# Kernel optimization log

Hardware: AMD Instinct MI355X
Metric: run time of the kernel (lower is better)

## Reference

```python
import jax, jax.numpy as jnp
import numpy as np


def blockdiag_matmul(x, w):
    """Block-diagonal (Monarch) linear: w has shape (nblocks, out_blk, in_blk);
    x has shape (..., nblocks*in_blk); returns (..., nblocks*out_blk)."""
    nb, q, p = w.shape
    lead = x.shape[:-1]
    xb = x.reshape(-1, nb, p)  # (tokens, nblocks, in_blk)
    out = jnp.einsum('bnp,nqp->bnq', xb, w)  # per-block matmul
    return out.reshape(*lead, nb * q)


def setup_inputs() -> dict:
    key = jax.random.key(0)
    k_x, k1, k2, k3 = jax.random.split(key, 4)
    B, S, D = 4, 4096, 2048
    NB, FF = 4, 8192  # nblocks, adjusted intermediate size
    # Kaiming-uniform-like scale for block weights (fan_in = D or FF per block-row)
    s1 = 1.0 / np.sqrt(D)
    s2 = 1.0 / np.sqrt(FF)
    return {
        'x': jax.random.normal(k_x, (B, S, D), dtype=jnp.float32),
        'w1': jax.random.normal(k1, (NB, FF // NB, D // NB), dtype=jnp.float32) * s1,
        'w3': jax.random.normal(k3, (NB, FF // NB, D // NB), dtype=jnp.float32) * s1,
        'w2': jax.random.normal(k2, (NB, D // NB, FF // NB), dtype=jnp.float32) * s2,
    }


def reference(x, w1, w3, w2):
    # SwiGLU MLP: w2(silu(w1(x)) * w3(x)), all projections block-diagonal
    gate = jax.nn.silu(blockdiag_matmul(x, w1))
    up = blockdiag_matmul(x, w3)
    return blockdiag_matmul(gate * up, w2)
```

## Files before the change

kernel.cpp:

```cpp
#include <hip/hip_runtime.h>
#include <cstdint>

typedef __attribute__((ext_vector_type(8))) short bf16x8;
typedef __attribute__((ext_vector_type(4))) float f32x4;
typedef unsigned short u16;

#define RD(p) (*(const bf16x8*)(p))

__device__ inline u16 f2bf(float f) {
  union { float f; unsigned int u; } v; v.f = f;
  unsigned int u = v.u;
  unsigned int r = (u + 0x7fffu + ((u >> 16) & 1u)) >> 16;
  return (u16)r;
}

__device__ inline void gload_lds16(const u16* g, u16* l) {
  __builtin_amdgcn_global_load_lds(
      (const __attribute__((address_space(1))) void*)g,
      (__attribute__((address_space(3))) void*)l, 16, 0, 0);
}

#define PH_BEGIN() \
  __builtin_amdgcn_s_barrier(); \
  asm volatile("s_waitcnt lgkmcnt(0)" ::: "memory"); \
  __builtin_amdgcn_s_setprio(1)
#define PH_END() \
  __builtin_amdgcn_s_setprio(0); \
  __builtin_amdgcn_s_barrier()

__global__ void cvt_f32_bf16(const float* __restrict__ src, u16* __restrict__ dst, int n8) {
  int i = blockIdx.x * blockDim.x + threadIdx.x;
  int stride = gridDim.x * blockDim.x;
  for (; i < n8; i += stride) {
    const float4* s = (const float4*)(src + (size_t)i * 8);
    float4 a = s[0], b = s[1];
    union { u16 h[8]; uint4 v; } o;
    o.h[0] = f2bf(a.x); o.h[1] = f2bf(a.y); o.h[2] = f2bf(a.z); o.h[3] = f2bf(a.w);
    o.h[4] = f2bf(b.x); o.h[5] = f2bf(b.y); o.h[6] = f2bf(b.z); o.h[7] = f2bf(b.w);
    *(uint4*)(dst + (size_t)i * 8) = o.v;
  }
}

__global__ void cvt_w3x(const float* __restrict__ s0, const float* __restrict__ s1,
                        const float* __restrict__ s2, u16* __restrict__ d0,
                        u16* __restrict__ d1, u16* __restrict__ d2) {
  const int n8 = 524288;
  int i = blockIdx.x * blockDim.x + threadIdx.x;
  int stride = gridDim.x * blockDim.x;
  for (; i < 3 * n8; i += stride) {
    int seg = i / n8;
    int j = i - seg * n8;
    const float* src = (seg == 0) ? s0 : (seg == 1) ? s1 : s2;
    u16* dst = (seg == 0) ? d0 : (seg == 1) ? d1 : d2;
    const float4* s = (const float4*)(src + (size_t)j * 8);
    float4 a = s[0], b = s[1];
    union { u16 h[8]; uint4 v; } o;
    o.h[0] = f2bf(a.x); o.h[1] = f2bf(a.y); o.h[2] = f2bf(a.z); o.h[3] = f2bf(a.w);
    o.h[4] = f2bf(b.x); o.h[5] = f2bf(b.y); o.h[6] = f2bf(b.z); o.h[7] = f2bf(b.w);
    *(uint4*)(dst + (size_t)j * 8) = o.v;
  }
}

__launch_bounds__(512, 2)
__global__ void gemm_gateup8(const u16* __restrict__ xb, const u16* __restrict__ w1b,
                             const u16* __restrict__ w3b, u16* __restrict__ hout) {
  constexpr int NT = 8;
  __shared__ __attribute__((aligned(16))) u16 lA[2][256 * 64];
  __shared__ __attribute__((aligned(16))) u16 lB[2][2][128 * 64];

  int bid = blockIdx.x;
  int sw = (bid & 7) * 512 + (bid >> 3);
  int nblk = sw >> 10;
  int rem = sw & 1023;
  int mt = rem >> 4, nt = rem & 15;

  int tid = threadIdx.x, w = tid >> 6, ln = tid & 63;
  int wr = w >> 1, wc = w & 1;
  int l15 = ln & 15, l4 = ln >> 4;
  int lr = ln >> 3, ln8 = ln & 7;

  int cx0 = ((l4 ^ (l15 & 7)) << 4);
  int cx1 = (((4 + l4) ^ (l15 & 7)) << 4);
  int aOff0 = (wr * 64 + l15) * 128 + cx0;
  int aOff1 = (wr * 64 + l15) * 128 + cx1;
  int bOff0 = (wc * 64 + l15) * 128 + cx0;
  int bOff1 = (wc * 64 + l15) * 128 + cx1;

  int u0t = w * 8, u1t = 64 + w * 8;
  int rbA0 = ((u0t >> 5) << 6) + (u0t & 31);
  int rbA1 = ((u1t >> 5) << 6) + (u1t & 31);
  int dA0 = rbA0 * 128, dA1 = rbA1 * 128;
  int dB0 = u0t * 128, dB1 = u1t * 128;
  int gaA0 = rbA0 * 2048, gaA1 = rbA1 * 2048;
  int gaB0 = u0t * 512, gaB1 = u1t * 512;
  int swzg = (ln8 ^ lr) << 3;

  const u16* gA  = xb  + (size_t)(mt * 256) * 2048 + nblk * 512 + lr * 2048 + swzg;
  const u16* gB1 = w1b + (size_t)nblk * (2048 * 512) + (size_t)(nt * 128) * 512 + lr * 512 + swzg;
  const u16* gB3 = w3b + (size_t)nblk * (2048 * 512) + (size_t)(nt * 128) * 512 + lr * 512 + swzg;

  f32x4 acc1[4][4], acc3[4][4];
#pragma unroll
  for (int i = 0; i < 4; i++)
#pragma unroll
    for (int j = 0; j < 4; j++) {
      acc1[i][j] = (f32x4){0.f, 0.f, 0.f, 0.f};
      acc3[i][j] = (f32x4){0.f, 0.f, 0.f, 0.f};
    }

  gload_lds16(gA + gaA0,          (u16*)((char*)lA + dA0));
  gload_lds16(gA + gaA1,          (u16*)((char*)lA + dA1));
  gload_lds16(gB3 + gaB0,         (u16*)((char*)lB + 16384 + dB0));
  gload_lds16(gB3 + gaB1,         (u16*)((char*)lB + 16384 + dB1));
  gload_lds16(gA + gaA0 + 65536,  (u16*)((char*)lA + dA0 + 4096));
  gload_lds16(gA + gaA1 + 65536,  (u16*)((char*)lA + dA1 + 4096));
  gload_lds16(gB1 + gaB0,         (u16*)((char*)lB + dB0));
  gload_lds16(gB1 + gaB1,         (u16*)((char*)lB + dB1));
  gload_lds16(gA + 64 + gaA0,         (u16*)((char*)lA + 32768 + dA0));
  gload_lds16(gA + 64 + gaA1,         (u16*)((char*)lA + 32768 + dA1));
  gload_lds16(gB3 + 64 + gaB0,        (u16*)((char*)lB + 32768 + 16384 + dB0));
  gload_lds16(gB3 + 64 + gaB1,        (u16*)((char*)lB + 32768 + 16384 + dB1));
  gload_lds16(gA + 64 + gaA0 + 65536, (u16*)((char*)lA + 32768 + dA0 + 4096));
  gload_lds16(gA + 64 + gaA1 + 65536, (u16*)((char*)lA + 32768 + dA1 + 4096));
  gA += 128; gB3 += 128; gB1 += 64;
  asm volatile("s_waitcnt vmcnt(6)" ::: "memory");
  __builtin_amdgcn_s_barrier();

  int sCur = 0, sNxt = 32768;
  bf16x8 aT[2][2], aH[2][2], b1[4][2], b3[4][2];

  for (int kt = 0; kt < NT; ++kt) {
    const char* pA0 = (const char*)lA + (sCur + aOff0);
    const char* pA1 = (const char*)lA + (sCur + aOff1);
    const char* pB0 = (const char*)lB + (sCur + bOff0);
    const char* pB1p = (const char*)lB + (sCur + bOff1);
    bool s1 = (kt + 1 < NT), s2 = (kt + 2 < NT);

#pragma unroll
    for (int f = 0; f < 2; ++f) {
      aT[f][0] = RD(pA0 + f * 2048); aT[f][1] = RD(pA1 + f * 2048);
    }
#pragma unroll
    for (int g = 0; g < 4; ++g) {
      b1[g][0] = RD(pB0 + g * 2048); b1[g][1] = RD(pB1p + g * 2048);
    }
    if (s1) {
      gload_lds16(gB1 + gaB0, (u16*)((char*)lB + sNxt + dB0));
      gload_lds16(gB1 + gaB1, (u16*)((char*)lB + sNxt + dB1));
    }
    asm volatile("s_waitcnt lgkmcnt(8)" ::: "memory");
    PH_BEGIN();
#pragma unroll
    for (int f = 0; f < 2; ++f)
#pragma unroll
      for (int g = 0; g < 4; ++g)
#pragma unroll
        for (int ks = 0; ks < 2; ++ks)
          acc1[f][g] = __builtin_amdgcn_mfma_f32_16x16x32_bf16(b1[g][ks], aT[f][ks], acc1[f][g], 0, 0, 0);
    PH_END();

#pragma unroll
    for (int g = 0; g < 4; ++g) {
      b3[g][0] = RD(pB0 + 16384 + g * 2048); b3[g][1] = RD(pB1p + 16384 + g * 2048);
    }
    if (s2) {
      gload_lds16(gA + gaA0, (u16*)((char*)lA + sCur + dA0));
      gload_lds16(gA + gaA1, (u16*)((char*)lA + sCur + dA1));
    }
    PH_BEGIN();
#pragma unroll
    for (int f = 0; f < 2; ++f)
#pragma unroll
      for (int g = 0; g < 4; ++g)
#pragma unroll
        for (int ks = 0; ks < 2; ++ks)
          acc3[f][g] = __builtin_amdgcn_mfma_f32_16x16x32_bf16(b3[g][ks], aT[f][ks], acc3[f][g], 0, 0, 0);
    PH_END();

#pragma unroll
    for (int f = 0; f < 2; ++f) {
      aH[f][0] = RD(pA0 + 4096 + f * 2048); aH[f][1] = RD(pA1 + 4096 + f * 2048);
    }
    if (s2) {
      gload_lds16(gB3 + gaB0, (u16*)((char*)lB + sCur + 16384 + dB0));
      gload_lds16(gB3 + gaB1, (u16*)((char*)lB + sCur + 16384 + dB1));
    }
    PH_BEGIN();
#pragma unroll
    for (int f = 0; f < 2; ++f)
#pragma unroll
      for (int g = 0; g < 4; ++g)
#pragma unroll
        for (int ks = 0; ks < 2; ++ks)
          acc1[2 + f][g] = __builtin_amdgcn_mfma_f32_16x16x32_bf16(b1[g][ks], aH[f][ks], acc1[2 + f][g], 0, 0, 0);
    PH_END();

    if (s2) {
      gload_lds16(gA + gaA0 + 65536, (u16*)((char*)lA + sCur + dA0 + 4096));
      gload_lds16(gA + gaA1 + 65536, (u16*)((char*)lA + sCur + dA1 + 4096));
    }
    PH_BEGIN();
#pragma unroll
    for (int f = 0; f < 2; ++f)
#pragma unroll
      for (int g = 0; g < 4; ++g)
#pragma unroll
        for (int ks = 0; ks < 2; ++ks)
          acc3[2 + f][g] = __builtin_amdgcn_mfma_f32_16x16x32_bf16(b3[g][ks], aH[f][ks], acc3[2 + f][g], 0, 0, 0);
    __builtin_amdgcn_s_setprio(0);
    if (kt < NT - 2)       asm volatile("s_waitcnt vmcnt(6)" ::: "memory");
    else if (kt == NT - 2) asm volatile("s_waitcnt vmcnt(0)" ::: "memory");
    __builtin_amdgcn_s_barrier();
    gA += 64; gB1 += 64; gB3 += 64;
    sCur ^= 32768; sNxt ^= 32768;
  }

  u16* Hb = hout + (size_t)(mt * 256 + wr * 64) * 8192 + nblk * 2048 + nt * 128 + wc * 64;
#pragma unroll
  for (int f = 0; f < 4; ++f) {
    u16* Hrow = Hb + (size_t)(f * 16 + l15) * 8192 + l4 * 4;
#pragma unroll
    for (int g = 0; g < 4; ++g) {
      union { u16 h[4]; unsigned long long v; } o;
#pragma unroll
      for (int r = 0; r < 4; ++r) {
        float gate = acc1[f][g][r];
        float up = acc3[f][g][r];
        float s = gate * __builtin_amdgcn_rcpf(1.f + __expf(-gate));
        o.h[r] = f2bf(s * up);
      }
      __builtin_nontemporal_store(o.v, (unsigned long long*)(Hrow + g * 16));
    }
  }
}

__launch_bounds__(512, 2)
__global__ void gemm_down8(const u16* __restrict__ hmat, const u16* __restrict__ w2b,
                           float* __restrict__ out) {
  constexpr int NT = 32;
  __shared__ __attribute__((aligned(16))) u16 lA[2][256 * 64];
  __shared__ __attribute__((aligned(16))) u16 lB[2][256 * 64];

  int bid = blockIdx.x;
  int sw = (bid & 7) * 64 + (bid >> 3);
  int nblk = sw >> 7;
  int rem = sw & 127;
  int mt = rem >> 1, nt = rem & 1;

  int tid = threadIdx.x, w = tid >> 6, ln = tid & 63;
  int mi = w >> 2, nj = w & 3;
  int l15 = ln & 15, l4 = ln >> 4;
  int lr = ln >> 3, ln8 = ln & 7;

  int cx0 = ((l4 ^ (l15 & 7)) << 4);
  int cx1 = (((4 + l4) ^ (l15 & 7)) << 4);
  int aOff0 = (mi * 128 + l15) * 128 + cx0;
  int aOff1 = (mi * 128 + l15) * 128 + cx1;
  int bOff0 = (nj * 64 + l15) * 128 + cx0;
  int bOff1 = (nj * 64 + l15) * 128 + cx1;

  int u0t = w * 8, u1t = 64 + w * 8;
  int dA0 = u0t * 128, dA1 = (64 + u1t) * 128;
  int rbB0 = ((u0t >> 5) << 6) + (u0t & 31);
  int rbB1 = ((u1t >> 5) << 6) + (u1t & 31);
  int dB0 = rbB0 * 128, dB1 = rbB1 * 128;
  int gaA0 = u0t * 8192, gaA1 = (64 + u1t) * 8192;
  int gaB0 = rbB0 * 2048, gaB1 = rbB1 * 2048;
  int swzg = (ln8 ^ lr) << 3;

  const u16* gA = hmat + (size_t)(mt * 256) * 8192 + nblk * 2048 + lr * 8192 + swzg;
  const u16* gB = w2b + (size_t)nblk * (512 * 2048) + (size_t)(nt * 256) * 2048 + lr * 2048 + swzg;

  f32x4 acc[8][4];
#pragma unroll
  for (int i = 0; i < 8; i++)
#pragma unroll
    for (int j = 0; j < 4; j++) acc[i][j] = (f32x4){0.f, 0.f, 0.f, 0.f};

  gload_lds16(gA + gaA0,           (u16*)((char*)lA + dA0));
  gload_lds16(gA + gaA1,           (u16*)((char*)lA + dA1));
  gload_lds16(gB + gaB0 + 65536,   (u16*)((char*)lB + dB0 + 4096));
  gload_lds16(gB + gaB1 + 65536,   (u16*)((char*)lB + dB1 + 4096));
  gload_lds16(gA + gaA0 + 524288,  (u16*)((char*)lA + dA0 + 8192));
  gload_lds16(gA + gaA1 + 524288,  (u16*)((char*)lA + dA1 + 8192));
  gload_lds16(gB + gaB0,           (u16*)((char*)lB + dB0));
  gload_lds16(gB + gaB1,           (u16*)((char*)lB + dB1));
  gload_lds16(gA + 64 + gaA0,          (u16*)((char*)lA + 32768 + dA0));
  gload_lds16(gA + 64 + gaA1,          (u16*)((char*)lA + 32768 + dA1));
  gload_lds16(gB + 64 + gaB0 + 65536,  (u16*)((char*)lB + 32768 + dB0 + 4096));
  gload_lds16(gB + 64 + gaB1 + 65536,  (u16*)((char*)lB + 32768 + dB1 + 4096));
  gload_lds16(gA + 64 + gaA0 + 524288, (u16*)((char*)lA + 32768 + dA0 + 8192));
  gload_lds16(gA + 64 + gaA1 + 524288, (u16*)((char*)lA + 32768 + dA1 + 8192));
  gA += 128; gB += 64;
  asm volatile("s_waitcnt vmcnt(6)" ::: "memory");
  __builtin_amdgcn_s_barrier();

  int sCur = 0, sNxt = 32768;
  bf16x8 aF[4][2], bLo[2][2], bHi[2][2];

  for (int kt = 0; kt < NT; ++kt) {
    const char* pA0 = (const char*)lA + (sCur + aOff0);
    const char* pA1 = (const char*)lA + (sCur + aOff1);
    const char* pB0 = (const char*)lB + (sCur + bOff0);
    const char* pB1p = (const char*)lB + (sCur + bOff1);
    bool s1 = (kt + 1 < NT), s2 = (kt + 2 < NT);

#pragma unroll
    for (int f = 0; f < 4; ++f) {
      aF[f][0] = RD(pA0 + f * 2048); aF[f][1] = RD(pA1 + f * 2048);
    }
#pragma unroll
    for (int g = 0; g < 2; ++g) {
      bLo[g][0] = RD(pB0 + g * 2048); bLo[g][1] = RD(pB1p + g * 2048);
    }
    if (s1) {
      gload_lds16(gB + gaB0, (u16*)((char*)lB + sNxt + dB0));
      gload_lds16(gB + gaB1, (u16*)((char*)lB + sNxt + dB1));
    }
    asm volatile("s_waitcnt lgkmcnt(8)" ::: "memory");
    PH_BEGIN();
#pragma unroll
    for (int f = 0; f < 4; ++f)
#pragma unroll
      for (int g = 0; g < 2; ++g)
#pragma unroll
        for (int ks = 0; ks < 2; ++ks)
          acc[f][g] = __builtin_amdgcn_mfma_f32_16x16x32_bf16(bLo[g][ks], aF[f][ks], acc[f][g], 0, 0, 0);
    PH_END();

#pragma unroll
    for (int g = 0; g < 2; ++g) {
      bHi[g][0] = RD(pB0 + 4096 + g * 2048); bHi[g][1] = RD(pB1p + 4096 + g * 2048);
    }
    if (s2) {
      gload_lds16(gA + gaA0, (u16*)((char*)lA + sCur + dA0));
      gload_lds16(gA + gaA1, (u16*)((char*)lA + sCur + dA1));
    }
    PH_BEGIN();
#pragma unroll
    for (int f = 0; f < 4; ++f)
#pragma unroll
      for (int g = 0; g < 2; ++g)
#pragma unroll
        for (int ks = 0; ks < 2; ++ks)
          acc[f][2 + g] = __builtin_amdgcn_mfma_f32_16x16x32_bf16(bHi[g][ks], aF[f][ks], acc[f][2 + g], 0, 0, 0);
    PH_END();

#pragma unroll
    for (int f = 0; f < 4; ++f) {
      aF[f][0] = RD(pA0 + 8192 + f * 2048); aF[f][1] = RD(pA1 + 8192 + f * 2048);
    }
    if (s2) {
      gload_lds16(gB + 64 + gaB0 + 65536, (u16*)((char*)lB + sCur + dB0 + 4096));
      gload_lds16(gB + 64 + gaB1 + 65536, (u16*)((char*)lB + sCur + dB1 + 4096));
    }
    PH_BEGIN();
#pragma unroll
    for (int f = 0; f < 4; ++f)
#pragma unroll
      for (int g = 0; g < 2; ++g)
#pragma unroll
        for (int ks = 0; ks < 2; ++ks)
          acc[4 + f][g] = __builtin_amdgcn_mfma_f32_16x16x32_bf16(bLo[g][ks], aF[f][ks], acc[4 + f][g], 0, 0, 0);
    PH_END();

    if (s2) {
      gload_lds16(gA + gaA0 + 524288, (u16*)((char*)lA + sCur + dA0 + 8192));
      gload_lds16(gA + gaA1 + 524288, (u16*)((char*)lA + sCur + dA1 + 8192));
    }
    PH_BEGIN();
#pragma unroll
    for (int f = 0; f < 4; ++f)
#pragma unroll
      for (int g = 0; g < 2; ++g)
#pragma unroll
        for (int ks = 0; ks < 2; ++ks)
          acc[4 + f][2 + g] = __builtin_amdgcn_mfma_f32_16x16x32_bf16(bHi[g][ks], aF[f][ks], acc[4 + f][2 + g], 0, 0, 0);
    __builtin_amdgcn_s_setprio(0);
    if (kt < NT - 2)       asm volatile("s_waitcnt vmcnt(6)" ::: "memory");
    else if (kt == NT - 2) asm volatile("s_waitcnt vmcnt(0)" ::: "memory");
    __builtin_amdgcn_s_barrier();
    gA += 64; gB += 64;
    sCur ^= 32768; sNxt ^= 32768;
  }

  float* Ob = out + (size_t)(mt * 256 + mi * 128) * 2048 + nblk * 512 + nt * 256 + nj * 64;
#pragma unroll
  for (int f = 0; f < 8; ++f) {
    float* Orow = Ob + (size_t)(f * 16 + l15) * 2048 + l4 * 4;
#pragma unroll
    for (int g = 0; g < 4; ++g)
      __builtin_nontemporal_store(acc[f][g], (f32x4*)(Orow + g * 16));
  }
}

extern "C" void kernel_launch(void* const* d_in, const int* in_sizes, int n_in,
                              void* d_out, int out_size, void* d_ws, size_t ws_size,
                              hipStream_t stream) {
  const float* x  = (const float*)d_in[0];
  const float* w1 = (const float*)d_in[1];
  const float* w3 = (const float*)d_in[2];
  const float* w2 = (const float*)d_in[3];

  char* ws = (char*)d_ws;
  u16* xb  = (u16*)(ws);
  u16* w1b = (u16*)(ws + 67108864);
  u16* w3b = (u16*)(ws + 75497472);
  u16* w2b = (u16*)(ws + 83886080);
  u16* h   = (u16*)(ws + 92274688);

  cvt_w3x<<<2048, 256, 0, stream>>>(w1, w3, w2, w1b, w3b, w2b);
  cvt_f32_bf16<<<2048, 256, 0, stream>>>(x, xb, 33554432 / 8);

  gemm_gateup8<<<4096, 512, 0, stream>>>(xb, w1b, w3b, h);
  gemm_down8<<<512, 512, 0, stream>>>(h, w2b, (float*)d_out);
}
```

Before: 591.7 us.

## Make gate/up GEMM persistent over four N-tiles with continuous pipeline

Each gate/up workgroup now handles four consecutive 128-wide N tiles, so the grid drops from 4096 to 1024 blocks. The double-buffered K pipeline runs unbroken across all 32 steps, and every 8 steps it writes the SiLU*up epilogue and clears the accumulators. The goal is to cut pipeline prologue/drain and launch/tail costs per tile. The A tile for each row block is now refetched per N tile from cache rather than reused, and nontemporal stores become plain stores in both kernels.

```diff
diff --git a/kernel.cpp b/kernel.cpp
--- a/kernel.cpp
+++ b/kernel.cpp
@@ -65,14 +65,16 @@
 __global__ void gemm_gateup8(const u16* __restrict__ xb, const u16* __restrict__ w1b,
                              const u16* __restrict__ w3b, u16* __restrict__ hout) {
   constexpr int NT = 8;
+  constexpr int TPB = 4;
+  constexpr int TOT = NT * TPB;
   __shared__ __attribute__((aligned(16))) u16 lA[2][256 * 64];
   __shared__ __attribute__((aligned(16))) u16 lB[2][2][128 * 64];
 
   int bid = blockIdx.x;
-  int sw = (bid & 7) * 512 + (bid >> 3);
-  int nblk = sw >> 10;
-  int rem = sw & 1023;
-  int mt = rem >> 4, nt = rem & 15;
+  int sw = (bid & 7) * 128 + (bid >> 3);
+  int nblk = sw >> 8;
+  int rem = sw & 255;
+  int mt = rem >> 2, ntg = rem & 3;
 
   int tid = threadIdx.x, w = tid >> 6, ln = tid & 63;
   int wr = w >> 1, wc = w & 1;
@@ -96,8 +98,11 @@
   int swzg = (ln8 ^ lr) << 3;
 
   const u16* gA  = xb  + (size_t)(mt * 256) * 2048 + nblk * 512 + lr * 2048 + swzg;
-  const u16* gB1 = w1b + (size_t)nblk * (2048 * 512) + (size_t)(nt * 128) * 512 + lr * 512 + swzg;
-  const u16* gB3 = w3b + (size_t)nblk * (2048 * 512) + (size_t)(nt * 128) * 512 + lr * 512 + swzg;
+  const u16* gB1 = w1b + (size_t)nblk * (2048 * 512) + (size_t)(ntg * 512) * 512 + lr * 512 + swzg;
+  const u16* gB3 = w3b + (size_t)nblk * (2048 * 512) + (size_t)(ntg * 512) * 512 + lr * 512 + swzg;
+
+  #define OFFA(s) (((s) & 7) * 64)
+  #define OFFB(s) ((((s) >> 3) << 16) + (((s) & 7) * 64))
 
   f32x4 acc1[4][4], acc3[4][4];
 #pragma unroll
@@ -108,33 +113,34 @@
       acc3[i][j] = (f32x4){0.f, 0.f, 0.f, 0.f};
     }
 
-  gload_lds16(gA + gaA0,          (u16*)((char*)lA + dA0));
-  gload_lds16(gA + gaA1,          (u16*)((char*)lA + dA1));
-  gload_lds16(gB3 + gaB0,         (u16*)((char*)lB + 16384 + dB0));
-  gload_lds16(gB3 + gaB1,         (u16*)((char*)lB + 16384 + dB1));
-  gload_lds16(gA + gaA0 + 65536,  (u16*)((char*)lA + dA0 + 4096));
-  gload_lds16(gA + gaA1 + 65536,  (u16*)((char*)lA + dA1 + 4096));
-  gload_lds16(gB1 + gaB0,         (u16*)((char*)lB + dB0));
-  gload_lds16(gB1 + gaB1,         (u16*)((char*)lB + dB1));
-  gload_lds16(gA + 64 + gaA0,         (u16*)((char*)lA + 32768 + dA0));
-  gload_lds16(gA + 64 + gaA1,         (u16*)((char*)lA + 32768 + dA1));
-  gload_lds16(gB3 + 64 + gaB0,        (u16*)((char*)lB + 32768 + 16384 + dB0));
-  gload_lds16(gB3 + 64 + gaB1,        (u16*)((char*)lB + 32768 + 16384 + dB1));
-  gload_lds16(gA + 64 + gaA0 + 65536, (u16*)((char*)lA + 32768 + dA0 + 4096));
-  gload_lds16(gA + 64 + gaA1 + 65536, (u16*)((char*)lA + 32768 + dA1 + 4096));
-  gA += 128; gB3 += 128; gB1 += 64;
+  gload_lds16(gA + gaA0,              (u16*)((char*)lA + dA0));
+  gload_lds16(gA + gaA1,              (u16*)((char*)lA + dA1));
+  gload_lds16(gB3 + gaB0,             (u16*)((char*)lB + 16384 + dB0));
+  gload_lds16(gB3 + gaB1,             (u16*)((char*)lB + 16384 + dB1));
+  gload_lds16(gA + gaA0 + 65536,      (u16*)((char*)lA + dA0 + 4096));
+  gload_lds16(gA + gaA1 + 65536,      (u16*)((char*)lA + dA1 + 4096));
+  gload_lds16(gB1 + gaB0,             (u16*)((char*)lB + dB0));
+  gload_lds16(gB1 + gaB1,             (u16*)((char*)lB + dB1));
+  gload_lds16(gA + OFFA(1) + gaA0,          (u16*)((char*)lA + 32768 + dA0));
+  gload_lds16(gA + OFFA(1) + gaA1,          (u16*)((char*)lA + 32768 + dA1));
+  gload_lds16(gB3 + OFFB(1) + gaB0,         (u16*)((char*)lB + 32768 + 16384 + dB0));
+  gload_lds16(gB3 + OFFB(1) + gaB1,         (u16*)((char*)lB + 32768 + 16384 + dB1));
+  gload_lds16(gA + OFFA(1) + gaA0 + 65536,  (u16*)((char*)lA + 32768 + dA0 + 4096));
+  gload_lds16(gA + OFFA(1) + gaA1 + 65536,  (u16*)((char*)lA + 32768 + dA1 + 4096));
   asm volatile("s_waitcnt vmcnt(6)" ::: "memory");
   __builtin_amdgcn_s_barrier();
 
   int sCur = 0, sNxt = 32768;
   bf16x8 aT[2][2], aH[2][2], b1[4][2], b3[4][2];
 
-  for (int kt = 0; kt < NT; ++kt) {
+  for (int kt = 0; kt < TOT; ++kt) {
     const char* pA0 = (const char*)lA + (sCur + aOff0);
     const char* pA1 = (const char*)lA + (sCur + aOff1);
     const char* pB0 = (const char*)lB + (sCur + bOff0);
     const char* pB1p = (const char*)lB + (sCur + bOff1);
-    bool s1 = (kt + 1 < NT), s2 = (kt + 2 < NT);
+    int s1 = kt + 1, s2 = kt + 2;
+    int oA2 = OFFA(s2), oB1n = OFFB(s1), oB32 = OFFB(s2);
+    bool q1 = (s1 < TOT), q2 = (s2 < TOT);
 
 #pragma unroll
     for (int f = 0; f < 2; ++f) {
@@ -144,9 +150,9 @@
     for (int g = 0; g < 4; ++g) {
       b1[g][0] = RD(pB0 + g * 2048); b1[g][1] = RD(pB1p + g * 2048);
     }
-    if (s1) {
-      gload_lds16(gB1 + gaB0, (u16*)((char*)lB + sNxt + dB0));
-      gload_lds16(gB1 + gaB1, (u16*)((char*)lB + sNxt + dB1));
+    if (q1) {
+      gload_lds16(gB1 + oB1n + gaB0, (u16*)((char*)lB + sNxt + dB0));
+      gload_lds16(gB1 + oB1n + gaB1, (u16*)((char*)lB + sNxt + dB1));
     }
     asm volatile("s_waitcnt lgkmcnt(8)" ::: "memory");
     PH_BEGIN();
@@ -163,9 +169,9 @@
     for (int g = 0; g < 4; ++g) {
       b3[g][0] = RD(pB0 + 16384 + g * 2048); b3[g][1] = RD(pB1p + 16384 + g * 2048);
     }
-    if (s2) {
-      gload_lds16(gA + gaA0, (u16*)((char*)lA + sCur + dA0));
-      gload_lds16(gA + gaA1, (u16*)((char*)lA + sCur + dA1));
+    if (q2) {
+      gload_lds16(gA + oA2 + gaA0, (u16*)((char*)lA + sCur + dA0));
+      gload_lds16(gA + oA2 + gaA1, (u16*)((char*)lA + sCur + dA1));
     }
     PH_BEGIN();
 #pragma unroll
@@ -181,9 +187,9 @@
     for (int f = 0; f < 2; ++f) {
       aH[f][0] = RD(pA0 + 4096 + f * 2048); aH[f][1] = RD(pA1 + 4096 + f * 2048);
     }
-    if (s2) {
-      gload_lds16(gB3 + gaB0, (u16*)((char*)lB + sCur + 16384 + dB0));
-      gload_lds16(gB3 + gaB1, (u16*)((char*)lB + sCur + 16384 + dB1));
+    if (q2) {
+      gload_lds16(gB3 + oB32 + gaB0, (u16*)((char*)lB + sCur + 16384 + dB0));
+      gload_lds16(gB3 + oB32 + gaB1, (u16*)((char*)lB + sCur + 16384 + dB1));
     }
     PH_BEGIN();
 #pragma unroll
@@ -195,9 +201,9 @@
           acc1[2 + f][g] = __builtin_amdgcn_mfma_f32_16x16x32_bf16(b1[g][ks], aH[f][ks], acc1[2 + f][g], 0, 0, 0);
     PH_END();
 
-    if (s2) {
-      gload_lds16(gA + gaA0 + 65536, (u16*)((char*)lA + sCur + dA0 + 4096));
-      gload_lds16(gA + gaA1 + 65536, (u16*)((char*)lA + sCur + dA1 + 4096));
+    if (q2) {
+      gload_lds16(gA + oA2 + gaA0 + 65536, (u16*)((char*)lA + sCur + dA0 + 4096));
+      gload_lds16(gA + oA2 + gaA1 + 65536, (u16*)((char*)lA + sCur + dA1 + 4096));
     }
     PH_BEGIN();
 #pragma unroll
@@ -208,30 +214,41 @@
         for (int ks = 0; ks < 2; ++ks)
           acc3[2 + f][g] = __builtin_amdgcn_mfma_f32_16x16x32_bf16(b3[g][ks], aH[f][ks], acc3[2 + f][g], 0, 0, 0);
     __builtin_amdgcn_s_setprio(0);
-    if (kt < NT - 2)       asm volatile("s_waitcnt vmcnt(6)" ::: "memory");
-    else if (kt == NT - 2) asm volatile("s_waitcnt vmcnt(0)" ::: "memory");
+    if (kt < TOT - 2)       asm volatile("s_waitcnt vmcnt(6)" ::: "memory");
+    else if (kt == TOT - 2) asm volatile("s_waitcnt vmcnt(0)" ::: "memory");
     __builtin_amdgcn_s_barrier();
-    gA += 64; gB1 += 64; gB3 += 64;
     sCur ^= 32768; sNxt ^= 32768;
+
+    if ((kt & 7) == 7) {
+      int nt = ntg * 4 + (kt >> 3);
+      u16* Hb = hout + (size_t)(mt * 256 + wr * 64) * 8192 + nblk * 2048 + nt * 128 + wc * 64;
+#pragma unroll
+      for (int f = 0; f < 4; ++f) {
+        u16* Hrow = Hb + (size_t)(f * 16 + l15) * 8192 + l4 * 4;
+#pragma unroll
+        for (int g = 0; g < 4; ++g) {
+          union { u16 h[4]; uint2 v; } o;
+#pragma unroll
+          for (int r = 0; r < 4; ++r) {
+            float gate = acc1[f][g][r];
+            float up = acc3[f][g][r];
+            float s = gate * __builtin_amdgcn_rcpf(1.f + __expf(-gate));
+            o.h[r] = f2bf(s * up);
+          }
+          *(uint2*)(Hrow + g * 16) = o.v;
+        }
+      }
+#pragma unroll
+      for (int i = 0; i < 4; i++)
+#pragma unroll
+        for (int j = 0; j < 4; j++) {
+          acc1[i][j] = (f32x4){0.f, 0.f, 0.f, 0.f};
+          acc3[i][j] = (f32x4){0.f, 0.f, 0.f, 0.f};
+        }
+    }
   }
-
-  u16* Hb = hout + (size_t)(mt * 256 + wr * 64) * 8192 + nblk * 2048 + nt * 128 + wc * 64;
-#pragma unroll
-  for (int f = 0; f < 4; ++f) {
-    u16* Hrow = Hb + (size_t)(f * 16 + l15) * 8192 + l4 * 4;
-#pragma unroll
-    for (int g = 0; g < 4; ++g) {
-      union { u16 h[4]; unsigned long long v; } o;
-#pragma unroll
-      for (int r = 0; r < 4; ++r) {
-        float gate = acc1[f][g][r];
-        float up = acc3[f][g][r];
-        float s = gate * __builtin_amdgcn_rcpf(1.f + __expf(-gate));
-        o.h[r] = f2bf(s * up);
-      }
-      __builtin_nontemporal_store(o.v, (unsigned long long*)(Hrow + g * 16));
-    }
-  }
+  #undef OFFA
+  #undef OFFB
 }
 
 __launch_bounds__(512, 2)
@@ -390,7 +407,7 @@
     float* Orow = Ob + (size_t)(f * 16 + l15) * 2048 + l4 * 4;
 #pragma unroll
     for (int g = 0; g < 4; ++g)
-      __builtin_nontemporal_store(acc[f][g], (f32x4*)(Orow + g * 16));
+      *(f32x4*)(Orow + g * 16) = acc[f][g];
   }
 }
 
@@ -412,6 +429,6 @@
   cvt_w3x<<<2048, 256, 0, stream>>>(w1, w3, w2, w1b, w3b, w2b);
   cvt_f32_bf16<<<2048, 256, 0, stream>>>(x, xb, 33554432 / 8);
 
-  gemm_gateup8<<<4096, 512, 0, stream>>>(xb, w1b, w3b, h);
+  gemm_gateup8<<<1024, 512, 0, stream>>>(xb, w1b, w3b, h);
   gemm_down8<<<512, 512, 0, stream>>>(h, w2b, (float*)d_out);
 }
```

New measurement: 569.0 us. -3.8%, faster.
